# Optimization experiments

Measured on AMD Instinct MI355X. Metric: run time of the kernel, lower is better.

Reference implementation:

```python
import jax, jax.numpy as jnp
import numpy as np

N = 50000
F_IN = 256
H1, D1 = 8, 8            # conv1: 8 heads x 8 dims, concat -> 64
H2, C = 8, 16            # conv2: 8 heads x num_classes, concat -> 128
NEG_SLOPE = 0.2


def setup_inputs() -> dict:
    key = jax.random.key(0)
    ks = jax.random.split(key, 10)
    x = jax.random.normal(ks[0], (N, F_IN), dtype=jnp.float32)
    edge_index = jax.random.randint(ks[1], (2, 800000), 0, N, dtype=jnp.int64)
    s1 = 1.0 / np.sqrt(F_IN)
    s2 = 1.0 / np.sqrt(H1 * D1)
    return {
        "x": x,
        "edge_index": edge_index,
        "W1": jax.random.normal(ks[2], (F_IN, H1 * D1), dtype=jnp.float32) * s1,
        "a1_src": jax.random.normal(ks[3], (H1, D1), dtype=jnp.float32) * s2,
        "a1_dst": jax.random.normal(ks[4], (H1, D1), dtype=jnp.float32) * s2,
        "b1": jnp.zeros((H1 * D1,), dtype=jnp.float32),
        "W2": jax.random.normal(ks[5], (H1 * D1, H2 * C), dtype=jnp.float32) * s2,
        "a2_src": jax.random.normal(ks[6], (H2, C), dtype=jnp.float32) * (1.0 / np.sqrt(C)),
        "a2_dst": jax.random.normal(ks[7], (H2, C), dtype=jnp.float32) * (1.0 / np.sqrt(C)),
        "b2": jnp.zeros((H2 * C,), dtype=jnp.float32),
    }


def _add_self_loops(edge_index, n):
    loops = jnp.arange(n, dtype=edge_index.dtype)
    return jnp.concatenate([edge_index, jnp.stack([loops, loops])], axis=1)


def _gat_conv(x, src, dst, W, a_src, a_dst, b, heads, out_dim, n):
    # xw: [N, H, O]
    xw = (x @ W).reshape(n, heads, out_dim)
    al_src = jnp.einsum("nho,ho->nh", xw, a_src)  # [N, H]
    al_dst = jnp.einsum("nho,ho->nh", xw, a_dst)
    e = jax.nn.leaky_relu(al_src[src] + al_dst[dst], NEG_SLOPE)  # [E, H]
    # segment softmax over edges sharing a destination node
    e_max = jax.ops.segment_max(e, dst, num_segments=n)
    e_exp = jnp.exp(e - e_max[dst])
    denom = jax.ops.segment_sum(e_exp, dst, num_segments=n)
    alpha = e_exp / (denom[dst] + 1e-16)                          # [E, H]
    msg = xw[src] * alpha[:, :, None]                              # [E, H, O]
    out = jax.ops.segment_sum(msg, dst, num_segments=n)           # [N, H, O]
    return out.reshape(n, heads * out_dim) + b, alpha


def reference(x, edge_index, W1, a1_src, a1_dst, b1, W2, a2_src, a2_dst, b2):
    ei = _add_self_loops(edge_index, N)
    src, dst = ei[0], ei[1]
    # dropout is a no-op at inference (training=False)
    h1, alpha1 = _gat_conv(x, src, dst, W1, a1_src, a1_dst, b1, H1, D1, N)
    h1 = jax.nn.elu(h1)
    h2, _ = _gat_conv(h1, src, dst, W2, a2_src, a2_dst, b2, H2, C, N)
    logp = jax.nn.log_softmax(h2, axis=1)
    return logp, alpha1
```

## Files before the change

### kernel.cpp

```cpp
#include <hip/hip_runtime.h>

#define N_NODES 50000
#define N_EDGES 800000
#define N_TOT   850000
#define NEG 0.2f
#define ELLW 64

#define G1_TILES 782
#define G2_TILES 782

#define NBIN   250
#define NPBIN  200
#define BKBLK  200
#define EPBK   4000
#define BCAP   32
#define OCAP   4096

__device__ __forceinline__ float leaky(float x) { return fmaxf(x, NEG * x); }

__device__ __forceinline__ unsigned bf16pk(float a, float b) {
  unsigned ua = __float_as_uint(a), ub = __float_as_uint(b);
  ua = (ua + 0x7FFFu + ((ua >> 16) & 1u)) >> 16;
  ub = (ub + 0x7FFFu + ((ub >> 16) & 1u)) >> 16;
  return ua | (ub << 16);
}
__device__ __forceinline__ float blo(unsigned u) { return __uint_as_float(u << 16); }
__device__ __forceinline__ float bhi(unsigned u) { return __uint_as_float(u & 0xFFFF0000u); }
__device__ __forceinline__ float bh2f(unsigned short h) { return __uint_as_float(((unsigned)h) << 16); }

__device__ __forceinline__ unsigned sel8(uint4 A, unsigned e) {
  unsigned w = (e & 4) ? ((e & 2) ? A.w : A.z) : ((e & 2) ? A.y : A.x);
  return (e & 1) ? (w >> 16) : (w & 0xFFFFu);
}

__global__ __launch_bounds__(256) void bin_gemm1_k(const float* __restrict__ x,
    const float* __restrict__ W1, const float* __restrict__ a1sv, const float* __restrict__ a1dv,
    unsigned short* __restrict__ xw1h, float* __restrict__ al1s, float* __restrict__ a1dd,
    const int* __restrict__ srcA, const int* __restrict__ dstA,
    unsigned* __restrict__ slots, unsigned short* __restrict__ bcnt2,
    unsigned* __restrict__ ofl, int* __restrict__ ofc)
{
  __shared__ __align__(16) char smem[33024];
  const int t = threadIdx.x;
  if (blockIdx.x < BKBLK) {
    unsigned (*buf)[BCAP] = (unsigned(*)[BCAP])smem;
    int* bc = (int*)(smem + 32000);
    for (int k = t; k < NBIN; k += 256) bc[k] = 0;
    __syncthreads();
    const int e0 = blockIdx.x * EPBK;
#pragma unroll
    for (int j = 0; j < 4; ++j) {
      int i4 = j * 256 + t;
      if (i4 < EPBK / 4) {
        int4 s4 = ((const int4*)(srcA + e0))[i4];
        int4 d4 = ((const int4*)(dstA + e0))[i4];
        int dd[4] = {d4.x, d4.y, d4.z, d4.w};
        int ss[4] = {s4.x, s4.y, s4.z, s4.w};
#pragma unroll
        for (int q = 0; q < 4; ++q) {
          int bin = dd[q] / NPBIN;
          unsigned rec = (unsigned)dd[q] | ((unsigned)ss[q] << 16);
          int p = atomicAdd(&bc[bin], 1);
          if (p < BCAP) buf[bin][p] = rec;
          else { int g = atomicAdd(ofc, 1); if (g < OCAP) ofl[g] = rec; }
        }
      }
    }
    __syncthreads();
    const int wv = t >> 6, ln = t & 63;
    for (int b = wv; b < NBIN; b += 4) {
      int c = bc[b]; if (c > BCAP) c = BCAP;
      if (ln == 0) bcnt2[(size_t)b * BKBLK + blockIdx.x] = (unsigned short)c;
      if (ln < c) slots[((size_t)b * BKBLK + blockIdx.x) * BCAP + ln] = buf[b][ln];
    }
    return;
  }
  float* xs  = (float*)smem;
  float* wsm = (float*)(smem + 8192);
  const int tx = t & 15, ty = t >> 4;
  const int n0 = (blockIdx.x - BKBLK) * 64;
  const int nl = t >> 2;
  const int ks = (t & 3) * 8;
  const int wk = t >> 3;
  const int wc = (t & 7) * 8;
  int gn = n0 + nl; if (gn >= N_NODES) gn = N_NODES - 1;
  const float* xrowb = x + (size_t)gn * 256 + ks;

  float acc[4][4];
#pragma unroll
  for (int r = 0; r < 4; ++r)
#pragma unroll
    for (int i = 0; i < 4; ++i) acc[r][i] = 0.f;

  float4 xv0, xv1, wv0, wv1;
  {
    const float4* xp = (const float4*)xrowb;
    xv0 = xp[0]; xv1 = xp[1];
    const float* wrow = W1 + (size_t)wk * 64 + wc;
    wv0 = ((const float4*)wrow)[0];
    wv1 = ((const float4*)wrow)[1];
  }
  for (int kc = 0; kc < 8; ++kc) {
    __syncthreads();
    xs[(ks + 0) * 64 + nl] = xv0.x;  xs[(ks + 1) * 64 + nl] = xv0.y;
    xs[(ks + 2) * 64 + nl] = xv0.z;  xs[(ks + 3) * 64 + nl] = xv0.w;
    xs[(ks + 4) * 64 + nl] = xv1.x;  xs[(ks + 5) * 64 + nl] = xv1.y;
    xs[(ks + 6) * 64 + nl] = xv1.z;  xs[(ks + 7) * 64 + nl] = xv1.w;
    ((float4*)&wsm[wk * 64 + wc])[0] = wv0;
    ((float4*)&wsm[wk * 64 + wc])[1] = wv1;
    __syncthreads();
    if (kc < 7) {
      const int kb = (kc + 1) * 32;
      const float4* xp = (const float4*)(xrowb + kb);
      xv0 = xp[0]; xv1 = xp[1];
      const float* wrow = W1 + (size_t)(kb + wk) * 64 + wc;
      wv0 = ((const float4*)wrow)[0];
      wv1 = ((const float4*)wrow)[1];
    }
#pragma unroll 4
    for (int k = 0; k < 32; ++k) {
      float4 xa = *(const float4*)&xs[k * 64 + ty * 4];
      float4 wv = *(const float4*)&wsm[k * 64 + tx * 4];
      float xn[4]; *(float4*)xn = xa;
      float wn[4]; *(float4*)wn = wv;
#pragma unroll
      for (int r = 0; r < 4; ++r)
#pragma unroll
        for (int i = 0; i < 4; ++i) acc[r][i] += xn[r] * wn[i];
    }
  }
  float cs[4], cd[4];
#pragma unroll
  for (int i = 0; i < 4; ++i) { cs[i] = a1sv[tx * 4 + i]; cd[i] = a1dv[tx * 4 + i]; }
#pragma unroll
  for (int r = 0; r < 4; ++r) {
    int n = n0 + ty * 4 + r;
    if (n >= N_NODES) break;
    uint2 pk;
    pk.x = bf16pk(acc[r][0], acc[r][1]);
    pk.y = bf16pk(acc[r][2], acc[r][3]);
    *(uint2*)(xw1h + (size_t)n * 64 + tx * 4) = pk;
    float ps = acc[r][0] * cs[0] + acc[r][1] * cs[1] + acc[r][2] * cs[2] + acc[r][3] * cs[3];
    float pd = acc[r][0] * cd[0] + acc[r][1] * cd[1] + acc[r][2] * cd[2] + acc[r][3] * cd[3];
    ps += __shfl_xor(ps, 1);
    pd += __shfl_xor(pd, 1);
    if ((tx & 1) == 0) {
      al1s[n * 8 + (tx >> 1)] = ps;
      a1dd[n * 16 + (tx >> 1)] = pd;
    }
  }
}

__global__ __launch_bounds__(256) void ell_k(const unsigned* __restrict__ slots,
    const unsigned short* __restrict__ bcnt2, const unsigned* __restrict__ ofl,
    const int* __restrict__ ofc, int* __restrict__ cnt, unsigned short* __restrict__ ell)
{
  __shared__ unsigned short ell_lds[NPBIN * ELLW];
  __shared__ int cnt_lds[NPBIN];
  const int t = threadIdx.x;
  const int b = blockIdx.x;
  for (int k = t; k < NPBIN; k += 256) cnt_lds[k] = 0;
  __syncthreads();
  if (t < BKBLK) {
    int c = bcnt2[(size_t)b * BKBLK + t];
    const uint4* sp4 = (const uint4*)(slots + ((size_t)b * BKBLK + t) * BCAP);
    uint4 R[8];
#pragma unroll
    for (int q = 0; q < 8; ++q) R[q] = sp4[q];
#pragma unroll
    for (int j = 0; j < BCAP; ++j) {
      if (j < c) {
        unsigned rec = ((const unsigned*)R)[j];
        int row = (int)(rec & 0xFFFFu) - b * NPBIN;
        int p = atomicAdd(&cnt_lds[row], 1);
        if (p < ELLW) ell_lds[row * ELLW + p] = (unsigned short)(rec >> 16);
      }
    }
  }
  __syncthreads();
  int oc = *ofc; if (oc > OCAP) oc = OCAP;
  for (int i = t; i < oc; i += 256) {
    unsigned rec = ofl[i];
    int d = rec & 0xFFFFu;
    if (d >= b * NPBIN && d < (b + 1) * NPBIN) {
      int p = atomicAdd(&cnt_lds[d - b * NPBIN], 1);
      if (p < ELLW) ell_lds[(d - b * NPBIN) * ELLW + p] = (unsigned short)(rec >> 16);
    }
  }
  __syncthreads();
  const uint4* s4 = (const uint4*)ell_lds;
  uint4* d4 = (uint4*)(ell + (size_t)b * NPBIN * ELLW);
  for (int i = t; i < NPBIN * ELLW / 8; i += 256) d4[i] = s4[i];
  for (int k = t; k < NPBIN; k += 256) cnt[b * NPBIN + k] = cnt_lds[k];
}

__global__ __launch_bounds__(256) void agg1_k(const unsigned short* __restrict__ xw1h,
    const float* __restrict__ al1s, float* __restrict__ a1dd,
    const int* __restrict__ cnt, const unsigned short* __restrict__ ell,
    const float* __restrict__ b1, float* __restrict__ h1)
{
  const unsigned lane = threadIdx.x & 63;
  const int n = blockIdx.x * 4 + (threadIdx.x >> 6);
  if (n >= N_NODES) return;
  const unsigned h = lane >> 3;
  const unsigned hw = lane & 7;
  const unsigned ew = lane >> 3;
  const float ad = a1dd[n * 16 + h];
  const float adH = __shfl(ad, (int)(hw << 3));
  float ws = __expf(leaky(al1s[n * 8 + h] + ad));
  float den0 = ws, den1 = 0.f;
  float acc0 = ws * bh2f(xw1h[(size_t)n * 64 + lane]), acc1 = 0.f;
  int num = cnt[n]; if (num > ELLW) num = ELLW;
  const uint4* cp = (const uint4*)(ell + (size_t)n * ELLW);
  int i = 0;
  for (; i + 8 <= num; i += 8) {
    uint4 A = cp[i >> 3];
    unsigned s0 = A.x & 0xFFFFu, s1 = A.x >> 16;
    unsigned s2 = A.y & 0xFFFFu, s3 = A.y >> 16;
    unsigned s4 = A.z & 0xFFFFu, s5 = A.z >> 16;
    unsigned s6 = A.w & 0xFFFFu, s7 = A.w >> 16;
    unsigned ssel = sel8(A, ew);
    float wv = __expf(leaky(al1s[(ssel << 3) + hw] + adH));
    float v0 = bh2f(xw1h[(s0 << 6) | lane]), v1 = bh2f(xw1h[(s1 << 6) | lane]);
    float v2 = bh2f(xw1h[(s2 << 6) | lane]), v3 = bh2f(xw1h[(s3 << 6) | lane]);
    float v4 = bh2f(xw1h[(s4 << 6) | lane]), v5 = bh2f(xw1h[(s5 << 6) | lane]);
    float v6 = bh2f(xw1h[(s6 << 6) | lane]), v7 = bh2f(xw1h[(s7 << 6) | lane]);
    float w0 = __shfl(wv, (int)(0 * 8 + h)), w1 = __shfl(wv, (int)(1 * 8 + h));
    float w2 = __shfl(wv, (int)(2 * 8 + h)), w3 = __shfl(wv, (int)(3 * 8 + h));
    float w4 = __shfl(wv, (int)(4 * 8 + h)), w5 = __shfl(wv, (int)(5 * 8 + h));
    float w6 = __shfl(wv, (int)(6 * 8 + h)), w7 = __shfl(wv, (int)(7 * 8 + h));
    acc0 += w0 * v0; acc1 += w1 * v1; acc0 += w2 * v2; acc1 += w3 * v3;
    acc0 += w4 * v4; acc1 += w5 * v5; acc0 += w6 * v6; acc1 += w7 * v7;
    den0 += w0 + w2 + w4 + w6; den1 += w1 + w3 + w5 + w7;
  }
  for (; i + 4 <= num; i += 4) {
    uint2 A = *(const uint2*)(ell + (size_t)n * ELLW + i);
    unsigned s0 = A.x & 0xFFFFu, s1 = A.x >> 16, s2 = A.y & 0xFFFFu, s3 = A.y >> 16;
    float l0 = al1s[(s0 << 3) + h] + ad, l1 = al1s[(s1 << 3) + h] + ad;
    float l2 = al1s[(s2 << 3) + h] + ad, l3 = al1s[(s3 << 3) + h] + ad;
    float v0 = bh2f(xw1h[(s0 << 6) | lane]), v1 = bh2f(xw1h[(s1 << 6) | lane]);
    float v2 = bh2f(xw1h[(s2 << 6) | lane]), v3 = bh2f(xw1h[(s3 << 6) | lane]);
    float w0 = __expf(leaky(l0)), w1 = __expf(leaky(l1));
    float w2 = __expf(leaky(l2)), w3 = __expf(leaky(l3));
    acc0 += w0 * v0; acc1 += w1 * v1; acc0 += w2 * v2; acc1 += w3 * v3;
    den0 += w0 + w2; den1 += w1 + w3;
  }
  for (; i < num; ++i) {
    unsigned s = ell[(size_t)n * ELLW + i];
    float w = __expf(leaky(al1s[(s << 3) + h] + ad));
    acc0 += w * bh2f(xw1h[(s << 6) | lane]);
    den0 += w;
  }
  float den = den0 + den1, acc = acc0 + acc1;
  if ((lane & 7) == 0) a1dd[n * 16 + 8 + h] = den;
  float o = acc / (den + 1e-16f) + b1[lane];
  h1[(size_t)n * 64 + lane] = o > 0.f ? o : (__expf(o) - 1.f);
}

__global__ __launch_bounds__(256) void gemm2_alpha_k(const float* __restrict__ h1,
    const float* __restrict__ W2, const float* __restrict__ a2sv, const float* __restrict__ a2dv,
    unsigned* __restrict__ xw2b, float* __restrict__ al2s, float* __restrict__ al2d,
    const int* __restrict__ srcA, const int* __restrict__ dstA,
    const float* __restrict__ al1s, const float* __restrict__ a1dd,
    float* __restrict__ alpha_out)
{
  __shared__ float xs[64 * 64];
  __shared__ float wsm[64 * 128];
  if (blockIdx.x >= G2_TILES) {
    int e = (blockIdx.x - G2_TILES) * 256 + threadIdx.x;
    if (e >= N_TOT) return;
    int s, d;
    if (e < N_EDGES) { s = srcA[e]; d = dstA[e]; }
    else             { s = d = e - N_EDGES; }
    float4 as0 = ((const float4*)(al1s + s * 8))[0];
    float4 as1 = ((const float4*)(al1s + s * 8))[1];
    const float4* dd = (const float4*)(a1dd + d * 16);
    float4 ad0 = dd[0];
    float4 ad1 = dd[1];
    float4 dn0 = dd[2];
    float4 dn1 = dd[3];
    float4 o0, o1;
    o0.x = __expf(leaky(as0.x + ad0.x)) / (dn0.x + 1e-16f);
    o0.y = __expf(leaky(as0.y + ad0.y)) / (dn0.y + 1e-16f);
    o0.z = __expf(leaky(as0.z + ad0.z)) / (dn0.z + 1e-16f);
    o0.w = __expf(leaky(as0.w + ad0.w)) / (dn0.w + 1e-16f);
    o1.x = __expf(leaky(as1.x + ad1.x)) / (dn1.x + 1e-16f);
    o1.y = __expf(leaky(as1.y + ad1.y)) / (dn1.y + 1e-16f);
    o1.z = __expf(leaky(as1.z + ad1.z)) / (dn1.z + 1e-16f);
    o1.w = __expf(leaky(as1.w + ad1.w)) / (dn1.w + 1e-16f);
    ((float4*)(alpha_out + (size_t)e * 8))[0] = o0;
    ((float4*)(alpha_out + (size_t)e * 8))[1] = o1;
    return;
  }
  const int t = threadIdx.x;
  const int tx = t & 15, ty = t >> 4;
  const int n0 = blockIdx.x * 64;
  {
    const int nl = t >> 2;
    const int ks = (t & 3) * 16;
    int gn = n0 + nl; if (gn >= N_NODES) gn = N_NODES - 1;
    const float4* hp = (const float4*)(h1 + (size_t)gn * 64 + ks);
#pragma unroll
    for (int j = 0; j < 4; ++j) {
      float4 v = hp[j];
      xs[(ks + 4 * j + 0) * 64 + nl] = v.x;
      xs[(ks + 4 * j + 1) * 64 + nl] = v.y;
      xs[(ks + 4 * j + 2) * 64 + nl] = v.z;
      xs[(ks + 4 * j + 3) * 64 + nl] = v.w;
    }
    const int wk = t >> 2;
    const int wc = (t & 3) * 32;
    const float4* wp = (const float4*)(W2 + (size_t)wk * 128 + wc);
    float4* wd = (float4*)&wsm[wk * 128 + wc];
#pragma unroll
    for (int j = 0; j < 8; ++j) wd[j] = wp[j];
  }
  __syncthreads();
  float acc[4][8];
#pragma unroll
  for (int r = 0; r < 4; ++r)
#pragma unroll
    for (int i = 0; i < 8; ++i) acc[r][i] = 0.f;
#pragma unroll 4
  for (int k = 0; k < 64; ++k) {
    float4 xa = *(const float4*)&xs[k * 64 + ty * 4];
    float4 wa = *(const float4*)&wsm[k * 128 + tx * 8];
    float4 wb = *(const float4*)&wsm[k * 128 + tx * 8 + 4];
    float xn[4]; *(float4*)xn = xa;
    float wn[8]; *(float4*)&wn[0] = wa; *(float4*)&wn[4] = wb;
#pragma unroll
    for (int r = 0; r < 4; ++r)
#pragma unroll
      for (int i = 0; i < 8; ++i) acc[r][i] += xn[r] * wn[i];
  }
  float cs[8], cd[8];
#pragma unroll
  for (int i = 0; i < 8; ++i) { cs[i] = a2sv[tx * 8 + i]; cd[i] = a2dv[tx * 8 + i]; }
#pragma unroll
  for (int r = 0; r < 4; ++r) {
    int n = n0 + ty * 4 + r;
    if (n >= N_NODES) break;
    uint4 pk;
    pk.x = bf16pk(acc[r][0], acc[r][1]);
    pk.y = bf16pk(acc[r][2], acc[r][3]);
    pk.z = bf16pk(acc[r][4], acc[r][5]);
    pk.w = bf16pk(acc[r][6], acc[r][7]);
    *(uint4*)(xw2b + (size_t)n * 64 + tx * 4) = pk;
    float ps = 0.f, pd = 0.f;
#pragma unroll
    for (int i = 0; i < 8; ++i) { ps += acc[r][i] * cs[i]; pd += acc[r][i] * cd[i]; }
    ps += __shfl_xor(ps, 1);
    pd += __shfl_xor(pd, 1);
    if ((tx & 1) == 0) {
      al2s[n * 8 + (tx >> 1)] = ps;
      al2d[n * 8 + (tx >> 1)] = pd;
    }
  }
}

__global__ __launch_bounds__(256) void agg2_k(const unsigned* __restrict__ xw2b,
    const float* __restrict__ al2s, const float* __restrict__ al2d,
    const int* __restrict__ cnt, const unsigned short* __restrict__ ell,
    const float* __restrict__ b2, float* __restrict__ logp)
{
  const unsigned lane = threadIdx.x & 63;
  const int n = blockIdx.x * 4 + (threadIdx.x >> 6);
  if (n >= N_NODES) return;
  const unsigned h = lane >> 3;
  const unsigned hw = lane & 7;
  const unsigned ew = lane >> 3;
  const float ad = al2d[n * 8 + h];
  const float adH = __shfl(ad, (int)(hw << 3));
  float ws = __expf(leaky(al2s[n * 8 + h] + ad));
  unsigned su = xw2b[(size_t)n * 64 + lane];
  float den0 = ws, den1 = 0.f;
  float ax0 = ws * blo(su), ay0 = ws * bhi(su), ax1 = 0.f, ay1 = 0.f;
  int num = cnt[n]; if (num > ELLW) num = ELLW;
  const uint4* cp = (const uint4*)(ell + (size_t)n * ELLW);
  int i = 0;
  for (; i + 8 <= num; i += 8) {
    uint4 A = cp[i >> 3];
    unsigned s0 = A.x & 0xFFFFu, s1 = A.x >> 16;
    unsigned s2 = A.y & 0xFFFFu, s3 = A.y >> 16;
    unsigned s4 = A.z & 0xFFFFu, s5 = A.z >> 16;
    unsigned s6 = A.w & 0xFFFFu, s7 = A.w >> 16;
    unsigned ssel = sel8(A, ew);
    float wv = __expf(leaky(al2s[(ssel << 3) + hw] + adH));
    unsigned u0 = xw2b[(s0 << 6) | lane], u1 = xw2b[(s1 << 6) | lane];
    unsigned u2 = xw2b[(s2 << 6) | lane], u3 = xw2b[(s3 << 6) | lane];
    unsigned u4 = xw2b[(s4 << 6) | lane], u5 = xw2b[(s5 << 6) | lane];
    unsigned u6 = xw2b[(s6 << 6) | lane], u7 = xw2b[(s7 << 6) | lane];
    float w0 = __shfl(wv, (int)(0 * 8 + h)), w1 = __shfl(wv, (int)(1 * 8 + h));
    float w2 = __shfl(wv, (int)(2 * 8 + h)), w3 = __shfl(wv, (int)(3 * 8 + h));
    float w4 = __shfl(wv, (int)(4 * 8 + h)), w5 = __shfl(wv, (int)(5 * 8 + h));
    float w6 = __shfl(wv, (int)(6 * 8 + h)), w7 = __shfl(wv, (int)(7 * 8 + h));
    ax0 += w0 * blo(u0); ay0 += w0 * bhi(u0);
    ax1 += w1 * blo(u1); ay1 += w1 * bhi(u1);
    ax0 += w2 * blo(u2); ay0 += w2 * bhi(u2);
    ax1 += w3 * blo(u3); ay1 += w3 * bhi(u3);
    ax0 += w4 * blo(u4); ay0 += w4 * bhi(u4);
    ax1 += w5 * blo(u5); ay1 += w5 * bhi(u5);
    ax0 += w6 * blo(u6); ay0 += w6 * bhi(u6);
    ax1 += w7 * blo(u7); ay1 += w7 * bhi(u7);
    den0 += w0 + w2 + w4 + w6; den1 += w1 + w3 + w5 + w7;
  }
  for (; i + 4 <= num; i += 4) {
    uint2 A = *(const uint2*)(ell + (size_t)n * ELLW + i);
    unsigned s0 = A.x & 0xFFFFu, s1 = A.x >> 16, s2 = A.y & 0xFFFFu, s3 = A.y >> 16;
    float l0 = al2s[(s0 << 3) + h] + ad, l1 = al2s[(s1 << 3) + h] + ad;
    float l2 = al2s[(s2 << 3) + h] + ad, l3 = al2s[(s3 << 3) + h] + ad;
    unsigned u0 = xw2b[(s0 << 6) | lane], u1 = xw2b[(s1 << 6) | lane];
    unsigned u2 = xw2b[(s2 << 6) | lane], u3 = xw2b[(s3 << 6) | lane];
    float w0 = __expf(leaky(l0)), w1 = __expf(leaky(l1));
    float w2 = __expf(leaky(l2)), w3 = __expf(leaky(l3));
    ax0 += w0 * blo(u0); ay0 += w0 * bhi(u0);
    ax1 += w1 * blo(u1); ay1 += w1 * bhi(u1);
    ax0 += w2 * blo(u2); ay0 += w2 * bhi(u2);
    ax1 += w3 * blo(u3); ay1 += w3 * bhi(u3);
    den0 += w0 + w2; den1 += w1 + w3;
  }
  for (; i < num; ++i) {
    unsigned s = ell[(size_t)n * ELLW + i];
    float w = __expf(leaky(al2s[(s << 3) + h] + ad));
    unsigned u = xw2b[(s << 6) | lane];
    ax0 += w * blo(u); ay0 += w * bhi(u); den0 += w;
  }
  float inv = 1.f / (den0 + den1 + 1e-16f);
  float o0 = (ax0 + ax1) * inv + b2[2 * lane];
  float o1 = (ay0 + ay1) * inv + b2[2 * lane + 1];
  float mx = fmaxf(o0, o1);
#pragma unroll
  for (int off = 1; off < 64; off <<= 1) mx = fmaxf(mx, __shfl_xor(mx, off));
  float se = __expf(o0 - mx) + __expf(o1 - mx);
#pragma unroll
  for (int off = 1; off < 64; off <<= 1) se += __shfl_xor(se, off);
  float lse = mx + __logf(se);
  float2 o; o.x = o0 - lse; o.y = o1 - lse;
  ((float2*)logp)[(size_t)n * 64 + lane] = o;
}

extern "C" void kernel_launch(void* const* d_in, const int* in_sizes, int n_in,
                              void* d_out, int out_size, void* d_ws, size_t ws_size,
                              hipStream_t stream)
{
  const float* x   = (const float*)d_in[0];
  const int*   ei  = (const int*)d_in[1];
  const float* W1  = (const float*)d_in[2];
  const float* a1s = (const float*)d_in[3];
  const float* a1d = (const float*)d_in[4];
  const float* b1  = (const float*)d_in[5];
  const float* W2  = (const float*)d_in[6];
  const float* a2s = (const float*)d_in[7];
  const float* a2d = (const float*)d_in[8];
  const float* b2  = (const float*)d_in[9];
  const int* srcA = ei;
  const int* dstA = ei + N_EDGES;

  char* ws = (char*)d_ws;
  unsigned short* xw1h = (unsigned short*)ws;            ws += (size_t)N_NODES * 64 * 2;
  float* h1    = (float*)ws;  ws += (size_t)N_NODES * 64 * 4;
  unsigned* xw2b = (unsigned*)ws; ws += (size_t)N_NODES * 64 * 4;
  float* al1s_ = (float*)ws;  ws += (size_t)N_NODES * 8 * 4;
  float* a1dd_ = (float*)ws;  ws += (size_t)N_NODES * 16 * 4;
  float* al2s_ = (float*)ws;  ws += (size_t)N_NODES * 8 * 4;
  float* al2d_ = (float*)ws;  ws += (size_t)N_NODES * 8 * 4;
  int* cnt    = (int*)ws;     ws += (size_t)N_NODES * 4;
  unsigned short* ell = (unsigned short*)ws; ws += (size_t)N_NODES * ELLW * 2;
  unsigned* slots = (unsigned*)ws; ws += (size_t)NBIN * BKBLK * BCAP * 4;
  unsigned short* bcnt2 = (unsigned short*)ws; ws += (size_t)NBIN * BKBLK * 2;
  unsigned* ofl = (unsigned*)ws; ws += (size_t)OCAP * 4;
  int* ofc = (int*)ws; ws += 16;

  float* logp      = (float*)d_out;
  float* alpha_out = logp + (size_t)N_NODES * 128;

  hipMemsetAsync(ofc, 0, sizeof(int), stream);

  bin_gemm1_k<<<BKBLK + G1_TILES, 256, 0, stream>>>(
      x, W1, a1s, a1d, xw1h, al1s_, a1dd_, srcA, dstA, slots, bcnt2, ofl, ofc);
  ell_k<<<NBIN, 256, 0, stream>>>(slots, bcnt2, ofl, ofc, cnt, ell);
  agg1_k<<<(N_NODES + 3) / 4, 256, 0, stream>>>(xw1h, al1s_, a1dd_, cnt, ell, b1, h1);
  gemm2_alpha_k<<<G2_TILES + (N_TOT + 255) / 256, 256, 0, stream>>>(
      h1, W2, a2s, a2d, xw2b, al2s_, al2d_, srcA, dstA, al1s_, a1dd_, alpha_out);
  agg2_k<<<(N_NODES + 3) / 4, 256, 0, stream>>>(xw2b, al2s_, al2d_, cnt, ell, b2, logp);
}
```

Before: 156.5 us.

## Enlarge GEMM1 tile to 256 nodes with 8x8 register blocking per thread

The first-layer GEMM now computes 256 node rows per block instead of 64. Each thread loads a full 32-wide x row slice and accumulates an 8x8 output micro-tile, which cuts the GEMM block count and raises the FMAs done per shared-memory load. Each thread's 8 outputs now cover exactly one head, so the attention dot products need no shuffle. In exchange it uses more registers (64 accumulators plus 8 float4 staging loads) and more shared memory, which may lower occupancy in the kernel it shares with the binning blocks, and the transposed x stores may bank-conflict.

```diff
diff --git a/kernel.cpp b/kernel.cpp
--- a/kernel.cpp
+++ b/kernel.cpp
@@ -6,7 +6,7 @@
 #define NEG 0.2f
 #define ELLW 64
 
-#define G1_TILES 782
+#define G1_TILES 196
 #define G2_TILES 782
 
 #define NBIN   250
@@ -40,7 +40,7 @@
     unsigned* __restrict__ slots, unsigned short* __restrict__ bcnt2,
     unsigned* __restrict__ ofl, int* __restrict__ ofc)
 {
-  __shared__ __align__(16) char smem[33024];
+  __shared__ __align__(16) char smem[40960];
   const int t = threadIdx.x;
   if (blockIdx.x < BKBLK) {
     unsigned (*buf)[BCAP] = (unsigned(*)[BCAP])smem;
@@ -76,78 +76,83 @@
     return;
   }
   float* xs  = (float*)smem;
-  float* wsm = (float*)(smem + 8192);
-  const int tx = t & 15, ty = t >> 4;
-  const int n0 = (blockIdx.x - BKBLK) * 64;
-  const int nl = t >> 2;
-  const int ks = (t & 3) * 8;
+  float* wsm = (float*)(smem + 32768);
+  const int tx = t & 7, ty = t >> 3;
+  const int n0 = (blockIdx.x - BKBLK) * 256;
   const int wk = t >> 3;
   const int wc = (t & 7) * 8;
-  int gn = n0 + nl; if (gn >= N_NODES) gn = N_NODES - 1;
-  const float* xrowb = x + (size_t)gn * 256 + ks;
-
-  float acc[4][4];
-#pragma unroll
-  for (int r = 0; r < 4; ++r)
-#pragma unroll
-    for (int i = 0; i < 4; ++i) acc[r][i] = 0.f;
-
-  float4 xv0, xv1, wv0, wv1;
+  int gn = n0 + t; if (gn >= N_NODES) gn = N_NODES - 1;
+  const float* xrow = x + (size_t)gn * 256;
+
+  float acc[8][8];
+#pragma unroll
+  for (int r = 0; r < 8; ++r)
+#pragma unroll
+    for (int i = 0; i < 8; ++i) acc[r][i] = 0.f;
+
+  float4 xv0, xv1, xv2, xv3, xv4, xv5, xv6, xv7, wv0, wv1;
   {
-    const float4* xp = (const float4*)xrowb;
-    xv0 = xp[0]; xv1 = xp[1];
+    const float4* xp = (const float4*)xrow;
+    xv0 = xp[0]; xv1 = xp[1]; xv2 = xp[2]; xv3 = xp[3];
+    xv4 = xp[4]; xv5 = xp[5]; xv6 = xp[6]; xv7 = xp[7];
     const float* wrow = W1 + (size_t)wk * 64 + wc;
     wv0 = ((const float4*)wrow)[0];
     wv1 = ((const float4*)wrow)[1];
   }
   for (int kc = 0; kc < 8; ++kc) {
     __syncthreads();
-    xs[(ks + 0) * 64 + nl] = xv0.x;  xs[(ks + 1) * 64 + nl] = xv0.y;
-    xs[(ks + 2) * 64 + nl] = xv0.z;  xs[(ks + 3) * 64 + nl] = xv0.w;
-    xs[(ks + 4) * 64 + nl] = xv1.x;  xs[(ks + 5) * 64 + nl] = xv1.y;
-    xs[(ks + 6) * 64 + nl] = xv1.z;  xs[(ks + 7) * 64 + nl] = xv1.w;
+    xs[ 0 * 256 + t] = xv0.x; xs[ 1 * 256 + t] = xv0.y; xs[ 2 * 256 + t] = xv0.z; xs[ 3 * 256 + t] = xv0.w;
+    xs[ 4 * 256 + t] = xv1.x; xs[ 5 * 256 + t] = xv1.y; xs[ 6 * 256 + t] = xv1.z; xs[ 7 * 256 + t] = xv1.w;
+    xs[ 8 * 256 + t] = xv2.x; xs[ 9 * 256 + t] = xv2.y; xs[10 * 256 + t] = xv2.z; xs[11 * 256 + t] = xv2.w;
+    xs[12 * 256 + t] = xv3.x; xs[13 * 256 + t] = xv3.y; xs[14 * 256 + t] = xv3.z; xs[15 * 256 + t] = xv3.w;
+    xs[16 * 256 + t] = xv4.x; xs[17 * 256 + t] = xv4.y; xs[18 * 256 + t] = xv4.z; xs[19 * 256 + t] = xv4.w;
+    xs[20 * 256 + t] = xv5.x; xs[21 * 256 + t] = xv5.y; xs[22 * 256 + t] = xv5.z; xs[23 * 256 + t] = xv5.w;
+    xs[24 * 256 + t] = xv6.x; xs[25 * 256 + t] = xv6.y; xs[26 * 256 + t] = xv6.z; xs[27 * 256 + t] = xv6.w;
+    xs[28 * 256 + t] = xv7.x; xs[29 * 256 + t] = xv7.y; xs[30 * 256 + t] = xv7.z; xs[31 * 256 + t] = xv7.w;
     ((float4*)&wsm[wk * 64 + wc])[0] = wv0;
     ((float4*)&wsm[wk * 64 + wc])[1] = wv1;
     __syncthreads();
     if (kc < 7) {
       const int kb = (kc + 1) * 32;
-      const float4* xp = (const float4*)(xrowb + kb);
-      xv0 = xp[0]; xv1 = xp[1];
+      const float4* xp = (const float4*)(xrow + kb);
+      xv0 = xp[0]; xv1 = xp[1]; xv2 = xp[2]; xv3 = xp[3];
+      xv4 = xp[4]; xv5 = xp[5]; xv6 = xp[6]; xv7 = xp[7];
       const float* wrow = W1 + (size_t)(kb + wk) * 64 + wc;
       wv0 = ((const float4*)wrow)[0];
       wv1 = ((const float4*)wrow)[1];
     }
-#pragma unroll 4
+#pragma unroll 2
     for (int k = 0; k < 32; ++k) {
-      float4 xa = *(const float4*)&xs[k * 64 + ty * 4];
-      float4 wv = *(const float4*)&wsm[k * 64 + tx * 4];
-      float xn[4]; *(float4*)xn = xa;
-      float wn[4]; *(float4*)wn = wv;
-#pragma unroll
-      for (int r = 0; r < 4; ++r)
-#pragma unroll
-        for (int i = 0; i < 4; ++i) acc[r][i] += xn[r] * wn[i];
-    }
-  }
-  float cs[4], cd[4];
-#pragma unroll
-  for (int i = 0; i < 4; ++i) { cs[i] = a1sv[tx * 4 + i]; cd[i] = a1dv[tx * 4 + i]; }
-#pragma unroll
-  for (int r = 0; r < 4; ++r) {
-    int n = n0 + ty * 4 + r;
+      float4 xa = *(const float4*)&xs[k * 256 + ty * 8];
+      float4 xb = *(const float4*)&xs[k * 256 + ty * 8 + 4];
+      float4 wa = *(const float4*)&wsm[k * 64 + tx * 8];
+      float4 wb = *(const float4*)&wsm[k * 64 + tx * 8 + 4];
+      float xn[8]; *(float4*)&xn[0] = xa; *(float4*)&xn[4] = xb;
+      float wn[8]; *(float4*)&wn[0] = wa; *(float4*)&wn[4] = wb;
+#pragma unroll
+      for (int r = 0; r < 8; ++r)
+#pragma unroll
+        for (int i = 0; i < 8; ++i) acc[r][i] += xn[r] * wn[i];
+    }
+  }
+  float cs[8], cd[8];
+#pragma unroll
+  for (int i = 0; i < 8; ++i) { cs[i] = a1sv[tx * 8 + i]; cd[i] = a1dv[tx * 8 + i]; }
+#pragma unroll
+  for (int r = 0; r < 8; ++r) {
+    int n = n0 + ty * 8 + r;
     if (n >= N_NODES) break;
-    uint2 pk;
+    uint4 pk;
     pk.x = bf16pk(acc[r][0], acc[r][1]);
     pk.y = bf16pk(acc[r][2], acc[r][3]);
-    *(uint2*)(xw1h + (size_t)n * 64 + tx * 4) = pk;
-    float ps = acc[r][0] * cs[0] + acc[r][1] * cs[1] + acc[r][2] * cs[2] + acc[r][3] * cs[3];
-    float pd = acc[r][0] * cd[0] + acc[r][1] * cd[1] + acc[r][2] * cd[2] + acc[r][3] * cd[3];
-    ps += __shfl_xor(ps, 1);
-    pd += __shfl_xor(pd, 1);
-    if ((tx & 1) == 0) {
-      al1s[n * 8 + (tx >> 1)] = ps;
-      a1dd[n * 16 + (tx >> 1)] = pd;
-    }
+    pk.z = bf16pk(acc[r][4], acc[r][5]);
+    pk.w = bf16pk(acc[r][6], acc[r][7]);
+    *(uint4*)(xw1h + (size_t)n * 64 + tx * 8) = pk;
+    float ps = 0.f, pd = 0.f;
+#pragma unroll
+    for (int i = 0; i < 8; ++i) { ps += acc[r][i] * cs[i]; pd += acc[r][i] * cd[i]; }
+    al1s[n * 8 + tx] = ps;
+    a1dd[n * 16 + tx] = pd;
   }
 }
 
```

Result: slower. 159.7 us (+2.0%).
